# Kernel tuning notes

Hardware: AMD Instinct MI355X
Metric: run time of the kernel (lower is better)

The kernel has to match this reference:

```python
import jax, jax.numpy as jnp
import numpy as np

B, DIN, H1, H2 = 16384, 512, 256, 128
S, DC, DE, T, TE, GH = 4, 4, 2, 3, 2, 64
NDOM = DC * DE            # 8 domain experts total
ETOT = S + NDOM + TE      # 14 experts feeding each task gate


def setup_inputs() -> dict:
    key = jax.random.key(0)
    ks = jax.random.split(key, 20)
    w = lambda k, shape, fan: (jax.random.normal(k, shape, jnp.float32) / np.sqrt(fan).astype(np.float32))
    x = jax.random.normal(ks[0], (B, DIN), jnp.float32)
    domain_ids = jax.random.randint(ks[1], (B,), 0, DC, jnp.int64) if jax.config.jax_enable_x64 else jax.random.randint(ks[1], (B,), 0, DC, jnp.int32)
    return {
        "x": x,
        "domain_ids": domain_ids,
        # shared experts (stacked): input->256->128, ReLU on both layers
        "sW1": w(ks[2], (S, DIN, H1), DIN), "sb1": jnp.zeros((S, H1), jnp.float32),
        "sW2": w(ks[3], (S, H1, H2), H1),   "sb2": jnp.zeros((S, H2), jnp.float32),
        # domain experts, all domains stacked in order domain0..domainDC-1
        "dW1": w(ks[4], (NDOM, DIN, H1), DIN), "db1": jnp.zeros((NDOM, H1), jnp.float32),
        "dW2": w(ks[5], (NDOM, H1, H2), H1),   "db2": jnp.zeros((NDOM, H2), jnp.float32),
        # task experts, all tasks stacked task0..taskT-1
        "tW1": w(ks[6], (T * TE, DIN, H1), DIN), "tb1": jnp.zeros((T * TE, H1), jnp.float32),
        "tW2": w(ks[7], (T * TE, H1, H2), H1),   "tb2": jnp.zeros((T * TE, H2), jnp.float32),
        # task gates (stacked over tasks): input->64 (ReLU) -> ETOT (linear) -> softmax
        "gW1": w(ks[8], (T, DIN, GH), DIN), "gb1": jnp.zeros((T, GH), jnp.float32),
        "gW2": w(ks[9], (T, GH, ETOT), GH), "gb2": jnp.zeros((T, ETOT), jnp.float32),
    }


def _experts(x, W1, b1, W2, b2):
    # x: [B, DIN]; W1: [E, DIN, H1]; W2: [E, H1, H2] -> [B, E, H2]
    h = jax.nn.relu(jnp.einsum('bi,eih->beh', x, W1) + b1)
    return jax.nn.relu(jnp.einsum('beh,eho->beo', h, W2) + b2)


def reference(x, domain_ids, sW1, sb1, sW2, sb2, dW1, db1, dW2, db2,
              tW1, tb1, tW2, tb2, gW1, gb1, gW2, gb2):
    shared = _experts(x, sW1, sb1, sW2, sb2)          # [B, S, H2]
    domain = _experts(x, dW1, db1, dW2, db2)          # [B, NDOM, H2]
    task = _experts(x, tW1, tb1, tW2, tb2)            # [B, T*TE, H2]
    task = task.reshape(B, T, TE, H2)
    base = jnp.concatenate([shared, domain], axis=1)  # [B, S+NDOM, H2]
    base = jnp.broadcast_to(base[:, None], (B, T, S + NDOM, H2))
    all_experts = jnp.concatenate([base, task], axis=2)  # [B, T, ETOT, H2]
    # task gates
    gh = jax.nn.relu(jnp.einsum('bi,tig->btg', x, gW1) + gb1)
    gates = jax.nn.softmax(jnp.einsum('btg,tge->bte', gh, gW2) + gb2, axis=-1)  # [B, T, ETOT]
    out = jnp.einsum('bteh,bte->tbh', all_experts, gates)  # [T, B, H2]
    # note: the torch per-sample domain_weighted_output is computed then discarded;
    # only these task outputs are returned, and they do not depend on domain_ids.
    return tuple(out[t] for t in range(T))
```

## Files before the change

### kernel.cpp

```cpp
#include <hip/hip_runtime.h>
#include <hip/hip_bf16.h>

#define NB 16384
#define DIN 512
#define H1 256
#define H2 128
#define NE 18
#define NT 3
#define NGH 64
#define NETOT 14

typedef float f32x4 __attribute__((ext_vector_type(4)));
typedef short s16x8 __attribute__((ext_vector_type(8)));
typedef unsigned short u16;
typedef unsigned int u32;

__device__ __forceinline__ u16 f2bf(float f) {
    union { float f; u32 u; } v; v.f = f;
    u32 r = v.u + 0x7fffu + ((v.u >> 16) & 1u);
    return (u16)(r >> 16);
}
__device__ __forceinline__ float bf2f(u16 u) {
    union { u32 u; float f; } v; v.u = ((u32)u) << 16;
    return v.f;
}
__device__ __forceinline__ u32 cvtpk(float a, float b) {
    u32 r;
    asm("v_cvt_pk_bf16_f32 %0, %1, %2" : "=v"(r) : "v"(a), "v"(b));
    return r;
}

#define GLDS16(g, l) __builtin_amdgcn_global_load_lds((const u32*)(g), (u32*)(l), 16, 0, 0)
#define VMCNT0_BARRIER() do { asm volatile("s_waitcnt vmcnt(0)" ::: "memory"); __builtin_amdgcn_s_barrier(); } while (0)

__global__ __launch_bounds__(256) void k_prep(
    const float* __restrict__ x, u16* __restrict__ xb,
    const float* __restrict__ sW1, const float* __restrict__ dW1, const float* __restrict__ tW1,
    const float* __restrict__ sW2, const float* __restrict__ dW2, const float* __restrict__ tW2,
    const float* __restrict__ gW1, u16* __restrict__ w1t, u16* __restrict__ w2t, u16* __restrict__ gw1t)
{
    __shared__ float lds[64 * 65];
    int bx = blockIdx.x;
    if (bx < 8192) {
        int i = (bx * 256 + threadIdx.x) * 4;
        float4 v = *reinterpret_cast<const float4*>(x + i);
        ushort4 o;
        o.x = f2bf(v.x); o.y = f2bf(v.y); o.z = f2bf(v.z); o.w = f2bf(v.w);
        *reinterpret_cast<ushort4*>(xb + i) = o;
        return;
    }
    int b = bx - 8192;
    const float* src; u16* dst; int K, N, k0, n0;
    if (b < 576) {
        int e = b >> 5, tile = b & 31;
        src = (e < 4) ? sW1 + (size_t)e * DIN * H1 : (e < 12) ? dW1 + (size_t)(e - 4) * DIN * H1
                                                              : tW1 + (size_t)(e - 12) * DIN * H1;
        dst = w1t + (size_t)e * H1 * DIN; K = DIN; N = H1;
        k0 = (tile >> 2) * 64; n0 = (tile & 3) * 64;
    } else if (b < 720) {
        int b2 = b - 576; int e = b2 >> 3, tile = b2 & 7;
        src = (e < 4) ? sW2 + (size_t)e * H1 * H2 : (e < 12) ? dW2 + (size_t)(e - 4) * H1 * H2
                                                             : tW2 + (size_t)(e - 12) * H1 * H2;
        dst = w2t + (size_t)e * H2 * H1; K = H1; N = H2;
        k0 = (tile >> 1) * 64; n0 = (tile & 1) * 64;
    } else {
        int b3 = b - 720; int t = b3 >> 3, tile = b3 & 7;
        src = gW1 + (size_t)t * DIN * NGH; dst = gw1t + (size_t)t * NGH * DIN; K = DIN; N = NGH;
        k0 = tile * 64; n0 = 0;
    }
    int t = threadIdx.x;
#pragma unroll
    for (int i = 0; i < 16; ++i) {
        int idx = i * 256 + t;
        int kk = idx >> 6, nn = idx & 63;
        lds[kk * 65 + nn] = src[(size_t)(k0 + kk) * N + n0 + nn];
    }
    __syncthreads();
#pragma unroll
    for (int i = 0; i < 16; ++i) {
        int idx = i * 256 + t;
        int nn = idx >> 6, kk = idx & 63;
        dst[(size_t)(n0 + nn) * K + k0 + kk] = f2bf(lds[kk * 65 + nn]);
    }
}

__global__ __launch_bounds__(512, 1) void k_expert_gate(
    const u16* __restrict__ xb, const u16* __restrict__ w1t, const u16* __restrict__ w2t,
    const float* __restrict__ sb1, const float* __restrict__ db1, const float* __restrict__ tb1,
    const float* __restrict__ sb2, const float* __restrict__ db2, const float* __restrict__ tb2,
    u16* __restrict__ eout,
    const u16* __restrict__ gw1t, const float* __restrict__ gb1,
    const float* __restrict__ gw2, const float* __restrict__ gb2, float* __restrict__ gates)
{
    __shared__ __align__(128) char smem[135168];

    const int bid = blockIdx.x;
    const int tid = threadIdx.x;
    const int w = tid >> 6, lane = tid & 63;
    const int l15 = lane & 15, q = lane >> 4;
    const int q16 = q * 16;

    if (bid >= 1152) {
        u16* xs  = reinterpret_cast<u16*>(smem);
        u16* g1s = reinterpret_cast<u16*>(smem) + 4608;
        float* ghs = reinterpret_cast<float*>(smem);

        int m0 = (bid - 1152) * 64;
        int wm = w & 1, wn = (w >> 1) & 1;
        int lk = q * 8, lr4 = q * 4;

        f32x4 acc[2][6];
#pragma unroll
        for (int i = 0; i < 2; ++i)
#pragma unroll
            for (int j = 0; j < 6; ++j) acc[i][j] = (f32x4)0.f;

        const u16* xg = xb + (size_t)m0 * DIN;
        const int srow = tid >> 3, su = (tid & 7) * 8;
        for (int kc = 0; kc < DIN / 64; ++kc) {
            *reinterpret_cast<uint4*>(&xs[srow * 72 + su]) =
                *reinterpret_cast<const uint4*>(xg + (size_t)srow * DIN + kc * 64 + su);
#pragma unroll
            for (int it = 0; it < 3; ++it) {
                int rr = it * 64 + srow;
                *reinterpret_cast<uint4*>(&g1s[rr * 72 + su]) =
                    *reinterpret_cast<const uint4*>(gw1t + (size_t)rr * DIN + kc * 64 + su);
            }
            __syncthreads();
            if (w < 4) {
                s16x8 af[2][2], bfr[6][2];
#pragma unroll
                for (int mi = 0; mi < 2; ++mi)
#pragma unroll
                    for (int kk = 0; kk < 2; ++kk)
                        af[mi][kk] = *reinterpret_cast<const s16x8*>(&xs[(wm * 32 + mi * 16 + l15) * 72 + kk * 32 + lk]);
#pragma unroll
                for (int nj = 0; nj < 6; ++nj)
#pragma unroll
                    for (int kk = 0; kk < 2; ++kk)
                        bfr[nj][kk] = *reinterpret_cast<const s16x8*>(&g1s[(wn * 96 + nj * 16 + l15) * 72 + kk * 32 + lk]);
#pragma unroll
                for (int kk = 0; kk < 2; ++kk)
#pragma unroll
                    for (int mi = 0; mi < 2; ++mi)
#pragma unroll
                        for (int nj = 0; nj < 6; ++nj)
                            acc[mi][nj] = __builtin_amdgcn_mfma_f32_16x16x32_bf16(af[mi][kk], bfr[nj][kk], acc[mi][nj], 0, 0, 0);
            }
            __syncthreads();
        }
        if (w < 4) {
#pragma unroll
            for (int mi = 0; mi < 2; ++mi)
#pragma unroll
                for (int nj = 0; nj < 6; ++nj) {
                    int col = wn * 96 + nj * 16 + l15;
                    float bias = gb1[col];
#pragma unroll
                    for (int r = 0; r < 4; ++r) {
                        int row = wm * 32 + mi * 16 + lr4 + r;
                        float v = acc[mi][nj][r] + bias;
                        ghs[row * 200 + col] = v > 0.f ? v : 0.f;
                    }
                }
        }
        __syncthreads();

        if (tid < 192) {
            int tt = tid >> 6, rr = tid & 63;
            float logit[NETOT];
#pragma unroll
            for (int e2 = 0; e2 < NETOT; ++e2) logit[e2] = gb2[tt * NETOT + e2];
            const float* g2 = gw2 + tt * NGH * NETOT;
            const float* gr = &ghs[rr * 200 + tt * 64];
            for (int g = 0; g < NGH; ++g) {
                float v = gr[g];
#pragma unroll
                for (int e2 = 0; e2 < NETOT; ++e2) logit[e2] += v * g2[g * NETOT + e2];
            }
            float m = logit[0];
#pragma unroll
            for (int e2 = 1; e2 < NETOT; ++e2) m = fmaxf(m, logit[e2]);
            float s = 0.f, p[NETOT];
#pragma unroll
            for (int e2 = 0; e2 < NETOT; ++e2) { p[e2] = __expf(logit[e2] - m); s += p[e2]; }
            float inv = 1.f / s;
            float* go = gates + (size_t)(m0 + rr) * (NT * NETOT) + tt * NETOT;
#pragma unroll
            for (int e2 = 0; e2 < NETOT; ++e2) go[e2] = p[e2] * inv;
        }
        return;
    }

    const int e  = bid >> 6;
    const int m0 = (bid & 63) * 256;
    const int wm = w >> 2, wn = w & 3;

    const u16* xg  = xb + (size_t)m0 * DIN;
    const u16* w1g = w1t + (size_t)e * H1 * DIN;
    const u16* w2g = w2t + (size_t)e * H2 * H1;
    const float* b1p = (e < 4) ? sb1 + e * H1 : (e < 12) ? db1 + (e - 4) * H1 : tb1 + (e - 12) * H1;
    const float* b2p = (e < 4) ? sb2 + e * H2 : (e < 12) ? db2 + (e - 4) * H2 : tb2 + (e - 12) * H2;

    const int srow8 = lane >> 3, sslot = lane & 7;
    const u16* gxa[4]; const u16* gxb[4]; int lxa[4], lxb[4];
#pragma unroll
    for (int j = 0; j < 4; ++j) {
        int baserow = w * 32 + j * 8, row = baserow + srow8;
        gxa[j] = xg  + (size_t)row * DIN + ((sslot ^ (row & 7)) * 8);
        gxb[j] = w1g + (size_t)row * DIN + ((sslot ^ (row & 7)) * 8);
        lxa[j] = baserow * 128;
        lxb[j] = 65536 + baserow * 128;
    }

    int offX[8], swA[8], offW[4], swB[4];
#pragma unroll
    for (int mi = 0; mi < 8; ++mi) {
        int r = wm * 128 + mi * 16 + l15;
        offX[mi] = r * 128; swA[mi] = (r & 7) << 4;
    }
#pragma unroll
    for (int nj = 0; nj < 4; ++nj) {
        int n = wn * 64 + nj * 16 + l15;
        offW[nj] = 65536 + n * 128; swB[nj] = (n & 7) << 4;
    }

    f32x4 acc1[8][4];
#pragma unroll
    for (int i = 0; i < 8; ++i)
#pragma unroll
        for (int j = 0; j < 4; ++j) acc1[i][j] = (f32x4)0.f;

#pragma unroll
    for (int j = 0; j < 4; ++j) GLDS16(gxa[j], smem + lxa[j]);
#pragma unroll
    for (int j = 0; j < 4; ++j) GLDS16(gxb[j], smem + lxb[j]);

    int buf = 0;
    for (int kt = 0; kt < 8; ++kt) {
        VMCNT0_BARRIER();
        if (kt < 7) {
            const int nb = (buf ^ 1) * 32768, ko = (kt + 1) * 64;
#pragma unroll
            for (int j = 0; j < 4; ++j) GLDS16(gxa[j] + ko, smem + nb + lxa[j]);
#pragma unroll
            for (int j = 0; j < 4; ++j) GLDS16(gxb[j] + ko, smem + nb + lxb[j]);
        }
        const int cb = buf * 32768;
#pragma unroll
        for (int kk = 0; kk < 2; ++kk) {
            const int kb = kk * 64 + q16;
            s16x8 wf[4];
#pragma unroll
            for (int nj = 0; nj < 4; ++nj)
                wf[nj] = *(const s16x8*)(smem + cb + offW[nj] + (kb ^ swB[nj]));
            {
                s16x8 xf[4];
#pragma unroll
                for (int i = 0; i < 4; ++i)
                    xf[i] = *(const s16x8*)(smem + cb + offX[i] + (kb ^ swA[i]));
                __builtin_amdgcn_s_setprio(1);
#pragma unroll
                for (int i = 0; i < 4; ++i)
#pragma unroll
                    for (int nj = 0; nj < 4; ++nj)
                        acc1[i][nj] = __builtin_amdgcn_mfma_f32_16x16x32_bf16(wf[nj], xf[i], acc1[i][nj], 0, 0, 0);
                __builtin_amdgcn_s_setprio(0);
            }
            __builtin_amdgcn_s_barrier();
            {
                s16x8 xf[4];
#pragma unroll
                for (int i = 0; i < 4; ++i)
                    xf[i] = *(const s16x8*)(smem + cb + offX[4 + i] + (kb ^ swA[4 + i]));
                __builtin_amdgcn_s_setprio(1);
#pragma unroll
                for (int i = 0; i < 4; ++i)
#pragma unroll
                    for (int nj = 0; nj < 4; ++nj)
                        acc1[4 + i][nj] = __builtin_amdgcn_mfma_f32_16x16x32_bf16(wf[nj], xf[i], acc1[4 + i][nj], 0, 0, 0);
                __builtin_amdgcn_s_setprio(0);
            }
            if (kk == 0) __builtin_amdgcn_s_barrier();
        }
        buf ^= 1;
    }
    __syncthreads();

#pragma unroll
    for (int mi = 0; mi < 8; ++mi) {
        const int m = wm * 128 + mi * 16 + l15;
        char* rowp = smem + m * 528;
#pragma unroll
        for (int nj = 0; nj < 4; ++nj) {
            const int n0 = wn * 64 + nj * 16 + q * 4;
            const float4 bv = *reinterpret_cast<const float4*>(b1p + n0);
            float v0 = fmaxf(acc1[mi][nj][0] + bv.x, 0.f);
            float v1 = fmaxf(acc1[mi][nj][1] + bv.y, 0.f);
            float v2 = fmaxf(acc1[mi][nj][2] + bv.z, 0.f);
            float v3 = fmaxf(acc1[mi][nj][3] + bv.w, 0.f);
            uint2 hv; hv.x = cvtpk(v0, v1); hv.y = cvtpk(v2, v3);
            *reinterpret_cast<uint2*>(rowp + n0 * 2) = hv;
        }
    }
    __syncthreads();

    f32x4 acc2[8][2];
#pragma unroll
    for (int i = 0; i < 8; ++i)
#pragma unroll
        for (int j = 0; j < 2; ++j) acc2[i][j] = (f32x4)0.f;
    const u16* w2p0 = w2g + (size_t)(wn * 32 + l15) * H1 + q * 8;
    const u16* w2p1 = w2g + (size_t)(wn * 32 + 16 + l15) * H1 + q * 8;
#pragma unroll
    for (int kt2 = 0; kt2 < 8; ++kt2) {
        s16x8 wf2[2], hf[8];
        wf2[0] = *(const s16x8*)(w2p0 + kt2 * 32);
        wf2[1] = *(const s16x8*)(w2p1 + kt2 * 32);
#pragma unroll
        for (int mi = 0; mi < 8; ++mi)
            hf[mi] = *(const s16x8*)(smem + (wm * 128 + mi * 16 + l15) * 528 + kt2 * 64 + q16);
#pragma unroll
        for (int mi = 0; mi < 8; ++mi)
#pragma unroll
            for (int pj = 0; pj < 2; ++pj)
                acc2[mi][pj] = __builtin_amdgcn_mfma_f32_16x16x32_bf16(hf[mi], wf2[pj], acc2[mi][pj], 0, 0, 0);
    }

    u16* eo = eout + ((size_t)e * NB + m0) * H2;
#pragma unroll
    for (int mi = 0; mi < 8; ++mi)
#pragma unroll
        for (int pj = 0; pj < 2; ++pj) {
            const int p = wn * 32 + pj * 16 + l15;
            const float bias = b2p[p];
#pragma unroll
            for (int r = 0; r < 4; ++r) {
                const int row = wm * 128 + mi * 16 + q * 4 + r;
                float v = acc2[mi][pj][r] + bias;
                eo[(size_t)row * H2 + p] = f2bf(v > 0.f ? v : 0.f);
            }
        }
}

__global__ __launch_bounds__(256) void k_combine(
    const u16* __restrict__ eout, const float* __restrict__ gates, float* __restrict__ out)
{
    int tid = threadIdx.x;
    int lr = tid >> 5, hq = tid & 31;
    int b = blockIdx.x * 8 + lr;
    int h0 = hq * 4;
    const float* g = gates + (size_t)b * (NT * NETOT);
    float o0[4] = {0, 0, 0, 0}, o1[4] = {0, 0, 0, 0}, o2[4] = {0, 0, 0, 0};
#pragma unroll
    for (int e = 0; e < NE; ++e) {
        ushort4 ev = *reinterpret_cast<const ushort4*>(&eout[((size_t)e * NB + b) * H2 + h0]);
        float v0 = bf2f(ev.x), v1 = bf2f(ev.y), v2 = bf2f(ev.z), v3 = bf2f(ev.w);
        if (e < 12) {
            float wa = g[e], wb = g[NETOT + e], wc = g[2 * NETOT + e];
            o0[0] += wa * v0; o0[1] += wa * v1; o0[2] += wa * v2; o0[3] += wa * v3;
            o1[0] += wb * v0; o1[1] += wb * v1; o1[2] += wb * v2; o1[3] += wb * v3;
            o2[0] += wc * v0; o2[1] += wc * v1; o2[2] += wc * v2; o2[3] += wc * v3;
        } else {
            int t = (e - 12) >> 1, te = (e - 12) & 1;
            float wt = g[t * NETOT + 12 + te];
            float* ot = (t == 0) ? o0 : (t == 1) ? o1 : o2;
            ot[0] += wt * v0; ot[1] += wt * v1; ot[2] += wt * v2; ot[3] += wt * v3;
        }
    }
    size_t base = (size_t)b * H2 + h0;
    *reinterpret_cast<float4*>(&out[0 * (size_t)NB * H2 + base]) = make_float4(o0[0], o0[1], o0[2], o0[3]);
    *reinterpret_cast<float4*>(&out[1 * (size_t)NB * H2 + base]) = make_float4(o1[0], o1[1], o1[2], o1[3]);
    *reinterpret_cast<float4*>(&out[2 * (size_t)NB * H2 + base]) = make_float4(o2[0], o2[1], o2[2], o2[3]);
}

extern "C" void kernel_launch(void* const* d_in, const int* in_sizes, int n_in,
                              void* d_out, int out_size, void* d_ws, size_t ws_size,
                              hipStream_t stream)
{
    const float* x   = (const float*)d_in[0];
    const float* sW1 = (const float*)d_in[2];
    const float* sb1 = (const float*)d_in[3];
    const float* sW2 = (const float*)d_in[4];
    const float* sb2 = (const float*)d_in[5];
    const float* dW1 = (const float*)d_in[6];
    const float* db1 = (const float*)d_in[7];
    const float* dW2 = (const float*)d_in[8];
    const float* db2 = (const float*)d_in[9];
    const float* tW1 = (const float*)d_in[10];
    const float* tb1 = (const float*)d_in[11];
    const float* tW2 = (const float*)d_in[12];
    const float* tb2 = (const float*)d_in[13];
    const float* gW1 = (const float*)d_in[14];
    const float* gb1 = (const float*)d_in[15];
    const float* gW2 = (const float*)d_in[16];
    const float* gb2 = (const float*)d_in[17];

    char* ws = (char*)d_ws;
    u16*  xb    = (u16*)(ws + 0);
    u16*  w1t   = (u16*)(ws + 16777216);
    u16*  w2t   = (u16*)(ws + 21495808);
    u16*  gw1t  = (u16*)(ws + 22675456);
    float* gates = (float*)(ws + 22872064);
    u16*  eout  = (u16*)(ws + 25624576);

    k_prep<<<dim3(8936), dim3(256), 0, stream>>>(x, xb, sW1, dW1, tW1, sW2, dW2, tW2, gW1, w1t, w2t, gw1t);
    k_expert_gate<<<dim3(1408), dim3(512), 0, stream>>>(xb, w1t, w2t, sb1, db1, tb1, sb2, db2, tb2,
                                                        eout, gw1t, gb1, gW2, gb2, gates);
    k_combine<<<dim3(NB / 8), dim3(256), 0, stream>>>(eout, gates, (float*)d_out);
}
```

Measured before the change: 152.5 us.

## Restructure layer-1 GEMM mainloop into 4-stage K=32 pipeline with split A/B prefetch

Replaces the double-buffered K=64 tile loop with a four-slot ring of K=32 tiles, issuing three tiles ahead and interleaving the A and B global-to-LDS loads between MFMA half-steps. Partial vmcnt waits replace the full vmcnt(0) drain, so loads stay in flight across barriers. The LDS swizzle changes to suit 64-byte rows. It adds more barriers per K-step and carefully hand-counted wait values, which risk stalls or races if the counts are wrong.

```diff
diff --git a/kernel.cpp b/kernel.cpp
--- a/kernel.cpp
+++ b/kernel.cpp
@@ -31,7 +31,7 @@
 }
 
 #define GLDS16(g, l) __builtin_amdgcn_global_load_lds((const u32*)(g), (u32*)(l), 16, 0, 0)
-#define VMCNT0_BARRIER() do { asm volatile("s_waitcnt vmcnt(0)" ::: "memory"); __builtin_amdgcn_s_barrier(); } while (0)
+#define VMW(n) asm volatile("s_waitcnt vmcnt(" #n ")" ::: "memory")
 
 __global__ __launch_bounds__(256) void k_prep(
     const float* __restrict__ x, u16* __restrict__ xb,
@@ -202,27 +202,28 @@
     const float* b1p = (e < 4) ? sb1 + e * H1 : (e < 12) ? db1 + (e - 4) * H1 : tb1 + (e - 12) * H1;
     const float* b2p = (e < 4) ? sb2 + e * H2 : (e < 12) ? db2 + (e - 4) * H2 : tb2 + (e - 12) * H2;
 
-    const int srow8 = lane >> 3, sslot = lane & 7;
-    const u16* gxa[4]; const u16* gxb[4]; int lxa[4], lxb[4];
-#pragma unroll
-    for (int j = 0; j < 4; ++j) {
-        int baserow = w * 32 + j * 8, row = baserow + srow8;
-        gxa[j] = xg  + (size_t)row * DIN + ((sslot ^ (row & 7)) * 8);
-        gxb[j] = w1g + (size_t)row * DIN + ((sslot ^ (row & 7)) * 8);
-        lxa[j] = baserow * 128;
-        lxb[j] = 65536 + baserow * 128;
-    }
-
-    int offX[8], swA[8], offW[4], swB[4];
+    const int srow4 = lane >> 2, scol = lane & 3;
+    const u16* gA[2]; const u16* gB[2]; int lA[2], lB[2];
+#pragma unroll
+    for (int s = 0; s < 2; ++s) {
+        int row = s * 128 + w * 16 + srow4;
+        int sw = (scol ^ ((row >> 1) & 3)) * 8;
+        gA[s] = xg  + (size_t)row * DIN + sw;
+        gB[s] = w1g + (size_t)row * DIN + sw;
+        lA[s] = s * 8192 + w * 1024;
+        lB[s] = 16384 + s * 8192 + w * 1024;
+    }
+
+    int roffX[8], roffW[4];
 #pragma unroll
     for (int mi = 0; mi < 8; ++mi) {
         int r = wm * 128 + mi * 16 + l15;
-        offX[mi] = r * 128; swA[mi] = (r & 7) << 4;
+        roffX[mi] = r * 64 + (q16 ^ (((r >> 1) & 3) << 4));
     }
 #pragma unroll
     for (int nj = 0; nj < 4; ++nj) {
         int n = wn * 64 + nj * 16 + l15;
-        offW[nj] = 65536 + n * 128; swB[nj] = (n & 7) << 4;
+        roffW[nj] = 16384 + n * 64 + (q16 ^ (((n >> 1) & 3) << 4));
     }
 
     f32x4 acc1[8][4];
@@ -232,58 +233,83 @@
         for (int j = 0; j < 4; ++j) acc1[i][j] = (f32x4)0.f;
 
 #pragma unroll
-    for (int j = 0; j < 4; ++j) GLDS16(gxa[j], smem + lxa[j]);
-#pragma unroll
-    for (int j = 0; j < 4; ++j) GLDS16(gxb[j], smem + lxb[j]);
-
-    int buf = 0;
-    for (int kt = 0; kt < 8; ++kt) {
-        VMCNT0_BARRIER();
-        if (kt < 7) {
-            const int nb = (buf ^ 1) * 32768, ko = (kt + 1) * 64;
-#pragma unroll
-            for (int j = 0; j < 4; ++j) GLDS16(gxa[j] + ko, smem + nb + lxa[j]);
-#pragma unroll
-            for (int j = 0; j < 4; ++j) GLDS16(gxb[j] + ko, smem + nb + lxb[j]);
-        }
-        const int cb = buf * 32768;
-#pragma unroll
-        for (int kk = 0; kk < 2; ++kk) {
-            const int kb = kk * 64 + q16;
-            s16x8 wf[4];
+    for (int u = 0; u < 3; ++u) {
+        const int ub = u * 32768, ko = u * 32;
+        GLDS16(gA[0] + ko, smem + ub + lA[0]); GLDS16(gA[1] + ko, smem + ub + lA[1]);
+        GLDS16(gB[0] + ko, smem + ub + lB[0]); GLDS16(gB[1] + ko, smem + ub + lB[1]);
+    }
+
+#pragma unroll
+    for (int i = 0; i < 8; ++i) {
+        const int cb0 = ((2 * i) & 3) * 32768;
+        const int cb1 = ((2 * i + 1) & 3) * 32768;
+        s16x8 af[8], bf[4];
+
+        if (i <= 6) {
+            const int u = 2 * i + 3, ub = (u & 3) * 32768, ko = u * 32;
+            GLDS16(gA[0] + ko, smem + ub + lA[0]); GLDS16(gA[1] + ko, smem + ub + lA[1]);
+        }
+        if (i < 7) { VMW(10); } else { VMW(4); }
+        __builtin_amdgcn_s_barrier();
+#pragma unroll
+        for (int mi = 0; mi < 8; ++mi) af[mi] = *(const s16x8*)(smem + cb0 + roffX[mi]);
+#pragma unroll
+        for (int nj = 0; nj < 4; ++nj) bf[nj] = *(const s16x8*)(smem + cb0 + roffW[nj]);
+        __builtin_amdgcn_s_setprio(1);
+#pragma unroll
+        for (int mi = 0; mi < 4; ++mi)
 #pragma unroll
             for (int nj = 0; nj < 4; ++nj)
-                wf[nj] = *(const s16x8*)(smem + cb + offW[nj] + (kb ^ swB[nj]));
-            {
-                s16x8 xf[4];
-#pragma unroll
-                for (int i = 0; i < 4; ++i)
-                    xf[i] = *(const s16x8*)(smem + cb + offX[i] + (kb ^ swA[i]));
-                __builtin_amdgcn_s_setprio(1);
-#pragma unroll
-                for (int i = 0; i < 4; ++i)
-#pragma unroll
-                    for (int nj = 0; nj < 4; ++nj)
-                        acc1[i][nj] = __builtin_amdgcn_mfma_f32_16x16x32_bf16(wf[nj], xf[i], acc1[i][nj], 0, 0, 0);
-                __builtin_amdgcn_s_setprio(0);
-            }
-            __builtin_amdgcn_s_barrier();
-            {
-                s16x8 xf[4];
-#pragma unroll
-                for (int i = 0; i < 4; ++i)
-                    xf[i] = *(const s16x8*)(smem + cb + offX[4 + i] + (kb ^ swA[4 + i]));
-                __builtin_amdgcn_s_setprio(1);
-#pragma unroll
-                for (int i = 0; i < 4; ++i)
-#pragma unroll
-                    for (int nj = 0; nj < 4; ++nj)
-                        acc1[4 + i][nj] = __builtin_amdgcn_mfma_f32_16x16x32_bf16(wf[nj], xf[i], acc1[4 + i][nj], 0, 0, 0);
-                __builtin_amdgcn_s_setprio(0);
-            }
-            if (kk == 0) __builtin_amdgcn_s_barrier();
-        }
-        buf ^= 1;
+                acc1[mi][nj] = __builtin_amdgcn_mfma_f32_16x16x32_bf16(bf[nj], af[mi], acc1[mi][nj], 0, 0, 0);
+        __builtin_amdgcn_s_setprio(0);
+        __builtin_amdgcn_s_barrier();
+
+        if (i <= 6) {
+            const int u = 2 * i + 3, ub = (u & 3) * 32768, ko = u * 32;
+            GLDS16(gB[0] + ko, smem + ub + lB[0]); GLDS16(gB[1] + ko, smem + ub + lB[1]);
+        }
+        __builtin_amdgcn_s_barrier();
+        __builtin_amdgcn_s_setprio(1);
+#pragma unroll
+        for (int mi = 0; mi < 4; ++mi)
+#pragma unroll
+            for (int nj = 0; nj < 4; ++nj)
+                acc1[4 + mi][nj] = __builtin_amdgcn_mfma_f32_16x16x32_bf16(bf[nj], af[4 + mi], acc1[4 + mi][nj], 0, 0, 0);
+        __builtin_amdgcn_s_setprio(0);
+        __builtin_amdgcn_s_barrier();
+
+        if (i <= 5) {
+            const int u = 2 * i + 4, ub = (u & 3) * 32768, ko = u * 32;
+            GLDS16(gA[0] + ko, smem + ub + lA[0]); GLDS16(gA[1] + ko, smem + ub + lA[1]);
+        }
+        if (i < 6) { VMW(10); } else if (i == 6) { VMW(8); } else { VMW(0); }
+        __builtin_amdgcn_s_barrier();
+#pragma unroll
+        for (int mi = 0; mi < 8; ++mi) af[mi] = *(const s16x8*)(smem + cb1 + roffX[mi]);
+#pragma unroll
+        for (int nj = 0; nj < 4; ++nj) bf[nj] = *(const s16x8*)(smem + cb1 + roffW[nj]);
+        __builtin_amdgcn_s_setprio(1);
+#pragma unroll
+        for (int mi = 0; mi < 4; ++mi)
+#pragma unroll
+            for (int nj = 0; nj < 4; ++nj)
+                acc1[mi][nj] = __builtin_amdgcn_mfma_f32_16x16x32_bf16(bf[nj], af[mi], acc1[mi][nj], 0, 0, 0);
+        __builtin_amdgcn_s_setprio(0);
+        __builtin_amdgcn_s_barrier();
+
+        if (i <= 5) {
+            const int u = 2 * i + 4, ub = (u & 3) * 32768, ko = u * 32;
+            GLDS16(gB[0] + ko, smem + ub + lB[0]); GLDS16(gB[1] + ko, smem + ub + lB[1]);
+        }
+        __builtin_amdgcn_s_barrier();
+        __builtin_amdgcn_s_setprio(1);
+#pragma unroll
+        for (int mi = 0; mi < 4; ++mi)
+#pragma unroll
+            for (int nj = 0; nj < 4; ++nj)
+                acc1[4 + mi][nj] = __builtin_amdgcn_mfma_f32_16x16x32_bf16(bf[nj], af[4 + mi], acc1[4 + mi][nj], 0, 0, 0);
+        __builtin_amdgcn_s_setprio(0);
+        __builtin_amdgcn_s_barrier();
     }
     __syncthreads();
 
```

After: 152.0 us. About the same (-0.3%).
